# Optimization experiments

Hardware: AMD Instinct MI355X
Metric: run time of the kernel (lower is better)

Reference implementation:

```python
import jax, jax.numpy as jnp
import numpy as np

B, H, W, C, NH = 128, 14, 14, 768, 12
HD = C // NH  # 64
L = 2 * H - 1  # 27, rel pos table length


def setup_inputs() -> dict:
    key = jax.random.key(0)
    ks = jax.random.split(key, 6)
    return {
        "hidden_states": jax.random.normal(ks[0], (B, H, W, C), jnp.float32),
        "w_qkv": jax.random.normal(ks[1], (C, 3 * C), jnp.float32) * 0.02,
        "b_qkv": jnp.zeros((3 * C,), jnp.float32),
        "rel_pos_h": jax.random.normal(ks[2], (L, HD), jnp.float32) * 0.02,
        "rel_pos_w": jax.random.normal(ks[3], (L, HD), jnp.float32) * 0.02,
        "w_proj": jax.random.normal(ks[4], (C, C), jnp.float32) * 0.02,
        "b_proj": jnp.zeros((C,), jnp.float32),
    }


def _rel_table(size, rel_pos):
    # q_size == k_size -> coords = q - k + (size - 1), pure gather (no resize)
    coords = jnp.arange(size)[:, None] - jnp.arange(size)[None, :] + (size - 1)
    return rel_pos[coords]  # (size, size, HD)


def reference(hidden_states, w_qkv, b_qkv, rel_pos_h, rel_pos_w, w_proj, b_proj):
    scale = HD ** -0.5
    x = hidden_states.reshape(B, H * W, C)
    qkv = x @ w_qkv + b_qkv                                    # (B, HW, 3C)
    qkv = qkv.reshape(B, H * W, 3, NH, HD)
    qkv = jnp.transpose(qkv, (2, 0, 3, 1, 4)).reshape(3, B * NH, H * W, HD)
    q, k, v = qkv[0], qkv[1], qkv[2]                           # (B*NH, HW, HD)

    attn = jnp.einsum('bqd,bkd->bqk', q * scale, k)            # (B*NH, HW, HW)

    Rh = _rel_table(H, rel_pos_h)                              # (H, H, HD)
    Rw = _rel_table(W, rel_pos_w)                              # (W, W, HD)
    qr = q.reshape(B * NH, H, W, HD)
    rel_h = jnp.einsum('bhwc,hkc->bhwk', qr, Rh)               # (B*NH, H, W, H)
    rel_w = jnp.einsum('bhwc,wkc->bhwk', qr, Rw)               # (B*NH, H, W, W)

    attn = attn.reshape(B * NH, H, W, H, W)
    attn = attn + rel_h[..., :, None] + rel_w[..., None, :]
    attn = attn.reshape(B * NH, H * W, H * W)
    attn = jax.nn.softmax(attn, axis=-1)

    out = attn @ v                                             # (B*NH, HW, HD)
    out = out.reshape(B, NH, H, W, HD)
    out = jnp.transpose(out, (0, 2, 3, 1, 4)).reshape(B, H, W, C)
    return out @ w_proj + b_proj
```

## Files before the change

kernel.cpp:

```cpp
#include <hip/hip_runtime.h>

typedef __bf16 bf16_t;
typedef __bf16 bf16x8 __attribute__((ext_vector_type(8)));
typedef float floatx4 __attribute__((ext_vector_type(4)));

#define B_    128
#define H_    14
#define HW_   196
#define C_    768
#define NH_   12
#define HD_   64
#define M_    25088
#define NQKV_ 2304
#define KDIM_ 768
#define BK_   64
#define VPAD_ 208
#define RSTR  72
#define QSTR  104
#define PSTR  232
#define VSTR  224

__device__ __forceinline__ void async_cp16(const void* g, void* l) {
    __builtin_amdgcn_global_load_lds((const __attribute__((address_space(1))) void*)g,
                                     (__attribute__((address_space(3))) void*)l, 16, 0, 0);
}

__global__ __launch_bounds__(256) void cast_x_kernel(const float* __restrict__ in,
                                                     bf16_t* __restrict__ out) {
    size_t i = ((size_t)blockIdx.x * 256 + threadIdx.x) * 8;
    float4 a = *(const float4*)(in + i);
    float4 b = *(const float4*)(in + i + 4);
    bf16x8 v;
    v[0] = (bf16_t)a.x; v[1] = (bf16_t)a.y; v[2] = (bf16_t)a.z; v[3] = (bf16_t)a.w;
    v[4] = (bf16_t)b.x; v[5] = (bf16_t)b.y; v[6] = (bf16_t)b.z; v[7] = (bf16_t)b.w;
    *(bf16x8*)(out + i) = v;
}

__global__ __launch_bounds__(256) void transpose_cast_kernel(const float* __restrict__ in,
                                                             bf16_t* __restrict__ out,
                                                             int rows, int cols) {
    __shared__ float tile[32][33];
    int c0 = blockIdx.x * 32, r0 = blockIdx.y * 32;
    for (int i = threadIdx.y; i < 32; i += 8) {
        int r = r0 + i, c = c0 + threadIdx.x;
        if (r < rows && c < cols) tile[i][threadIdx.x] = in[(size_t)r * cols + c];
    }
    __syncthreads();
    for (int i = threadIdx.y; i < 32; i += 8) {
        int orow = c0 + i;
        int oc   = r0 + threadIdx.x;
        if (orow < cols && oc < rows)
            out[(size_t)orow * rows + oc] = (bf16_t)tile[threadIdx.x][i];
    }
}

__device__ __forceinline__ void gemm128_compute(const bf16_t* __restrict__ A,
                                                const bf16_t* __restrict__ Bt,
                                                int m0, int n0,
                                                floatx4 acc[4][4],
                                                bf16_t (*As)[BK_], bf16_t (*Bs)[BK_]) {
    const int tid  = threadIdx.x;
    const int lane = tid & 63, wave = tid >> 6;
    const int wm = (wave & 1) << 6, wn = (wave >> 1) << 6;
    const int lrow = lane & 15, quad = lane >> 4;

    #pragma unroll
    for (int i = 0; i < 4; i++)
        #pragma unroll
        for (int j = 0; j < 4; j++) acc[i][j] = (floatx4){0.f, 0.f, 0.f, 0.f};

    const int sr = tid >> 3;
    const int cc = tid & 7;

    for (int k0 = 0; k0 < KDIM_; k0 += BK_) {
        __syncthreads();
        #pragma unroll
        for (int i = 0; i < 4; i++) {
            int row  = sr + i * 32;
            int scol = ((cc ^ (row & 7)) * 8);
            async_cp16(A  + (size_t)(m0 + row) * KDIM_ + k0 + scol, &As[row][cc * 8]);
            async_cp16(Bt + (size_t)(n0 + row) * KDIM_ + k0 + scol, &Bs[row][cc * 8]);
        }
        __syncthreads();

        #pragma unroll
        for (int kh = 0; kh < 2; kh++) {
            bf16x8 af[4], bfr[4];
            #pragma unroll
            for (int i = 0; i < 4; i++) {
                int rw = wm + i * 16 + lrow;
                af[i] = *(const bf16x8*)&As[rw][((kh * 4 + quad) ^ (rw & 7)) * 8];
            }
            #pragma unroll
            for (int j = 0; j < 4; j++) {
                int rw = wn + j * 16 + lrow;
                bfr[j] = *(const bf16x8*)&Bs[rw][((kh * 4 + quad) ^ (rw & 7)) * 8];
            }
            #pragma unroll
            for (int i = 0; i < 4; i++)
                #pragma unroll
                for (int j = 0; j < 4; j++)
                    acc[i][j] = __builtin_amdgcn_mfma_f32_16x16x32_bf16(af[i], bfr[j], acc[i][j], 0, 0, 0);
        }
    }
}

__global__ __launch_bounds__(256) void qkv_gemm_kernel(const bf16_t* __restrict__ A,
                                                       const bf16_t* __restrict__ Bt,
                                                       const float* __restrict__ bias,
                                                       bf16_t* __restrict__ qb,
                                                       bf16_t* __restrict__ kb,
                                                       bf16_t* __restrict__ vtb) {
    __shared__ __align__(16) char smem[128 * 136 * 2];
    bf16_t (*As)[BK_] = (bf16_t(*)[BK_])smem;
    bf16_t (*Bs)[BK_] = (bf16_t(*)[BK_])(smem + 128 * BK_ * 2);
    bf16_t (*Cs)[136] = (bf16_t(*)[136])smem;

    const int lin = blockIdx.x;
    const int g = lin / 72, r = lin - g * 72;
    const int m0 = (g * 4 + (r & 3)) * 128;
    const int n0 = (r >> 2) * 128;
    floatx4 acc[4][4];
    gemm128_compute(A, Bt, m0, n0, acc, As, Bs);

    const int tid = threadIdx.x;
    const int lane = tid & 63, wave = tid >> 6;
    const int wm = (wave & 1) << 6, wn = (wave >> 1) << 6;
    const int lrow = lane & 15, quad = lane >> 4;
    const int sel = n0 / C_;

    if (sel == 2) {
        #pragma unroll
        for (int j = 0; j < 4; j++) {
            int n = n0 + wn + j * 16 + lrow;
            float bv = bias[n];
            int nc = n - 2 * C_;
            int nh = nc >> 6, hd = nc & 63;
            #pragma unroll
            for (int i = 0; i < 4; i++) {
                int m = m0 + wm + i * 16 + quad * 4;
                int b = m / HW_, t = m - b * HW_;
                int head = b * NH_ + nh;
                ushort4 pk;
                bf16_t h;
                h = (bf16_t)(acc[i][j][0] + bv); pk.x = __builtin_bit_cast(unsigned short, h);
                h = (bf16_t)(acc[i][j][1] + bv); pk.y = __builtin_bit_cast(unsigned short, h);
                h = (bf16_t)(acc[i][j][2] + bv); pk.z = __builtin_bit_cast(unsigned short, h);
                h = (bf16_t)(acc[i][j][3] + bv); pk.w = __builtin_bit_cast(unsigned short, h);
                *(ushort4*)(vtb + ((size_t)head * HD_ + hd) * VPAD_ + t) = pk;
            }
        }
    } else {
        const float sc = (sel == 0) ? 0.125f : 1.0f;
        __syncthreads();
        #pragma unroll
        for (int j = 0; j < 4; j++) {
            int n = n0 + wn + j * 16 + lrow;
            float bv = bias[n];
            #pragma unroll
            for (int i = 0; i < 4; i++)
                #pragma unroll
                for (int rr = 0; rr < 4; rr++)
                    Cs[wm + i * 16 + quad * 4 + rr][wn + j * 16 + lrow] =
                        (bf16_t)((acc[i][j][rr] + bv) * sc);
        }
        __syncthreads();
        bf16_t* dst = sel ? kb : qb;
        const int n0s = n0 - sel * C_;
        #pragma unroll
        for (int u = 0; u < 8; u++) {
            int idx = tid + u * 256;
            int rr = idx >> 4, c = idx & 15;
            int m = m0 + rr;
            int b = m / HW_, t = m - b * HW_;
            int ncol = n0s + c * 8;
            int nh = ncol >> 6, hd = ncol & 63;
            *(uint4*)(dst + (((size_t)(b * NH_ + nh)) * HW_ + t) * HD_ + hd) =
                *(const uint4*)&Cs[rr][c * 8];
        }
    }
}

__global__ __launch_bounds__(256) void proj_gemm_kernel(const bf16_t* __restrict__ A,
                                                        const bf16_t* __restrict__ Bt,
                                                        const float* __restrict__ bias,
                                                        float* __restrict__ out) {
    __shared__ __align__(16) bf16_t As[128][BK_];
    __shared__ __align__(16) bf16_t Bs[128][BK_];
    const int lin = blockIdx.x;
    const int g = lin / 24, r = lin - g * 24;
    const int m0 = (g * 4 + (r & 3)) * 128;
    const int n0 = (r >> 2) * 128;
    floatx4 acc[4][4];
    gemm128_compute(A, Bt, m0, n0, acc, As, Bs);

    const int lane = threadIdx.x & 63, wave = threadIdx.x >> 6;
    const int wm = (wave & 1) << 6, wn = (wave >> 1) << 6;
    const int lrow = lane & 15, quad = lane >> 4;
    #pragma unroll
    for (int j = 0; j < 4; j++) {
        int n = n0 + wn + j * 16 + lrow;
        float bv = bias[n];
        #pragma unroll
        for (int i = 0; i < 4; i++) {
            #pragma unroll
            for (int rr = 0; rr < 4; rr++) {
                int m = m0 + wm + i * 16 + quad * 4 + rr;
                out[(size_t)m * C_ + n] = acc[i][j][rr] + bv;
            }
        }
    }
}

__global__ __launch_bounds__(256, 3) void attn_kernel(const bf16_t* __restrict__ qb,
                                                      const bf16_t* __restrict__ kb,
                                                      const bf16_t* __restrict__ vtb,
                                                      const float* __restrict__ rph,
                                                      const float* __restrict__ rpw,
                                                      bf16_t* __restrict__ aout) {
    const int lin = blockIdx.x;
    const int task = (lin & 7) * 1344 + (lin >> 3);
    const int head = task / 7;
    const int qt = task - head * 7;
    const int bb = head / NH_, nh = head - bb * NH_;
    const int q0 = qt * 32;
    const int tid = threadIdx.x;
    const int lane = tid & 63, wave = tid >> 6;
    const int lrow = lane & 15, quad = lane >> 4;

    __shared__ __align__(16) bf16_t qs[32][QSTR];
    __shared__ __align__(16) bf16_t kvu[208 * QSTR];
    __shared__ __align__(16) bf16_t pbu[32 * PSTR];
    __shared__ bf16_t QRh[32][34];
    __shared__ bf16_t QRw[32][34];
    __shared__ float pmax[2][32], psum[2][32];

    bf16_t (*ks)[QSTR]  = (bf16_t(*)[QSTR])kvu;
    bf16_t (*vTs)[VSTR] = (bf16_t(*)[VSTR])kvu;
    bf16_t (*pb)[PSTR]  = (bf16_t(*)[PSTR])pbu;
    bf16_t (*rT)[RSTR]  = (bf16_t(*)[RSTR])pbu;

    bf16x8 z;
    #pragma unroll
    for (int e = 0; e < 8; e++) z[e] = (bf16_t)0.f;

    {
        int row = tid >> 3, col = (tid & 7) * 8;
        int t = q0 + row;
        *(bf16x8*)&qs[row][col] =
            (t < HW_) ? *(const bf16x8*)(qb + ((size_t)head * HW_ + t) * HD_ + col) : z;
    }
    #pragma unroll
    for (int t2 = 0; t2 < 2; t2++) {
        int u = tid * 2 + t2;
        int which = u >> 8, rem = u & 255;
        int l = rem >> 3, c = (rem & 7) * 8;
        bf16x8 v = z;
        if (l < 27) {
            const float* src = (which ? rpw : rph) + (size_t)l * HD_ + c;
            float4 a = *(const float4*)src;
            float4 b = *(const float4*)(src + 4);
            v[0] = (bf16_t)a.x; v[1] = (bf16_t)a.y; v[2] = (bf16_t)a.z; v[3] = (bf16_t)a.w;
            v[4] = (bf16_t)b.x; v[5] = (bf16_t)b.y; v[6] = (bf16_t)b.z; v[7] = (bf16_t)b.w;
        }
        *(bf16x8*)&rT[which * 32 + l][c] = v;
    }
    for (int v8 = tid; v8 < 208 * 8; v8 += 256) {
        int row = v8 >> 3, col = (v8 & 7) * 8;
        *(bf16x8*)&ks[row][col] =
            (row < HW_) ? *(const bf16x8*)(kb + ((size_t)head * HW_ + row) * HD_ + col) : z;
    }
    for (int u = tid; u < 208 * 5; u += 256) {
        int row = u / 5, c = u - row * 5;
        *(bf16x8*)&ks[row][64 + c * 8] = z;
    }
    __syncthreads();
    if (tid < 208 && tid < HW_) {
        int kh = tid / 14, kw = tid - kh * 14;
        ks[tid][64 + kh] = (bf16_t)1.0f;
        ks[tid][78 + kw] = (bf16_t)1.0f;
    }

    #pragma unroll
    for (int t2 = 0; t2 < 2; t2++) {
        int tsk = wave * 2 + t2;
        int which = tsk >> 2, mi2 = (tsk >> 1) & 1, ni = tsk & 1;
        floatx4 a4 = (floatx4){0.f, 0.f, 0.f, 0.f};
        #pragma unroll
        for (int kk = 0; kk < 2; kk++) {
            bf16x8 af  = *(const bf16x8*)&qs[mi2 * 16 + lrow][kk * 32 + quad * 8];
            bf16x8 bf8 = *(const bf16x8*)&rT[which * 32 + ni * 16 + lrow][kk * 32 + quad * 8];
            a4 = __builtin_amdgcn_mfma_f32_16x16x32_bf16(af, bf8, a4, 0, 0, 0);
        }
        int l = ni * 16 + lrow;
        if (l < 27) {
            bf16_t (*QR)[34] = which ? QRw : QRh;
            #pragma unroll
            for (int rr = 0; rr < 4; rr++) QR[mi2 * 16 + quad * 4 + rr][l] = (bf16_t)(a4[rr] * 8.f);
        }
    }
    __syncthreads();

    for (int u = tid; u < 1024; u += 256) {
        int row = u >> 5, kk = u & 31;
        int t = q0 + row;
        int h = t / 14, w = t - h * 14;
        bf16_t val = (bf16_t)0.f;
        if (kk < 14)      val = QRh[row][h - kk + 13];
        else if (kk < 28) val = QRw[row][w - (kk - 14) + 13];
        qs[row][64 + kk] = val;
    }
    if (tid < 96) {
        int row = tid / 3, col = 208 + (tid % 3) * 8;
        *(bf16x8*)&pb[row][col] = z;
    }
    __syncthreads();

    bf16x8 vstage[7];
    int vrow[7], vcol[7];
    #pragma unroll
    for (int i = 0; i < 7; i++) {
        int v8 = tid + i * 256;
        vrow[i] = v8 / 28;
        int c8 = v8 - vrow[i] * 28;
        vcol[i] = c8 * 8;
        vstage[i] = (vcol[i] < VPAD_)
            ? *(const bf16x8*)(vtb + ((size_t)head * HD_ + vrow[i]) * VPAD_ + vcol[i]) : z;
    }

    const int wh = wave >> 1, mi = wave & 1;
    const int NT = 7 - wh;
    float sv[7][4];
    float m4[4] = {-1e30f, -1e30f, -1e30f, -1e30f};
    for (int t = 0; t < NT; t++) {
        int jt = 2 * t + wh;
        floatx4 a4 = (floatx4){0.f, 0.f, 0.f, 0.f};
        #pragma unroll
        for (int kk = 0; kk < 3; kk++) {
            bf16x8 af  = *(const bf16x8*)&qs[mi * 16 + lrow][kk * 32 + quad * 8];
            bf16x8 bf8 = *(const bf16x8*)&ks[jt * 16 + lrow][kk * 32 + quad * 8];
            a4 = __builtin_amdgcn_mfma_f32_16x16x32_bf16(af, bf8, a4, 0, 0, 0);
        }
        int n = jt * 16 + lrow;
        bool valid = (n < HW_);
        #pragma unroll
        for (int rr = 0; rr < 4; rr++) {
            float s = valid ? a4[rr] : -1e30f;
            sv[t][rr] = s;
            m4[rr] = fmaxf(m4[rr], s);
        }
    }
    #pragma unroll
    for (int off = 1; off < 16; off <<= 1)
        #pragma unroll
        for (int rr = 0; rr < 4; rr++) m4[rr] = fmaxf(m4[rr], __shfl_xor(m4[rr], off));
    if (lrow == 0)
        #pragma unroll
        for (int rr = 0; rr < 4; rr++) pmax[wh][mi * 16 + quad * 4 + rr] = m4[rr];
    __syncthreads();

    float mxr[4], s4[4] = {0.f, 0.f, 0.f, 0.f};
    #pragma unroll
    for (int rr = 0; rr < 4; rr++) {
        int qi = mi * 16 + quad * 4 + rr;
        mxr[rr] = fmaxf(pmax[0][qi], pmax[1][qi]);
    }
    for (int t = 0; t < NT; t++) {
        int n = (2 * t + wh) * 16 + lrow;
        #pragma unroll
        for (int rr = 0; rr < 4; rr++) {
            float e = __expf(sv[t][rr] - mxr[rr]);
            s4[rr] += e;
            pb[mi * 16 + quad * 4 + rr][n] = (bf16_t)e;
        }
    }
    #pragma unroll
    for (int off = 1; off < 16; off <<= 1)
        #pragma unroll
        for (int rr = 0; rr < 4; rr++) s4[rr] += __shfl_xor(s4[rr], off);
    if (lrow == 0)
        #pragma unroll
        for (int rr = 0; rr < 4; rr++) psum[wh][mi * 16 + quad * 4 + rr] = s4[rr];
    #pragma unroll
    for (int i = 0; i < 7; i++) *(bf16x8*)&vTs[vrow[i]][vcol[i]] = vstage[i];
    __syncthreads();

    const int qit = wave & 1;
    const int qrow = qit * 16 + lrow;
    const float inv = 1.f / (psum[0][qrow] + psum[1][qrow]);
    const int t_out = q0 + qrow;
    #pragma unroll
    for (int jj = 0; jj < 2; jj++) {
        int hdt = (wave >> 1) * 2 + jj;
        floatx4 a4 = (floatx4){0.f, 0.f, 0.f, 0.f};
        #pragma unroll
        for (int kk = 0; kk < 7; kk++) {
            bf16x8 af  = *(const bf16x8*)&vTs[hdt * 16 + lrow][kk * 32 + quad * 8];
            bf16x8 bf8 = *(const bf16x8*)&pb[qit * 16 + lrow][kk * 32 + quad * 8];
            a4 = __builtin_amdgcn_mfma_f32_16x16x32_bf16(af, bf8, a4, 0, 0, 0);
        }
        if (t_out < HW_) {
            int col = nh * HD_ + hdt * 16 + quad * 4;
            ushort4 pk;
            bf16_t hv;
            hv = (bf16_t)(a4[0] * inv); pk.x = __builtin_bit_cast(unsigned short, hv);
            hv = (bf16_t)(a4[1] * inv); pk.y = __builtin_bit_cast(unsigned short, hv);
            hv = (bf16_t)(a4[2] * inv); pk.z = __builtin_bit_cast(unsigned short, hv);
            hv = (bf16_t)(a4[3] * inv); pk.w = __builtin_bit_cast(unsigned short, hv);
            *(ushort4*)(aout + ((size_t)bb * HW_ + t_out) * C_ + col) = pk;
        }
    }
}

extern "C" void kernel_launch(void* const* d_in, const int* in_sizes, int n_in,
                              void* d_out, int out_size, void* d_ws, size_t ws_size,
                              hipStream_t stream) {
    const float* hs    = (const float*)d_in[0];
    const float* wqkv  = (const float*)d_in[1];
    const float* bqkv  = (const float*)d_in[2];
    const float* rph   = (const float*)d_in[3];
    const float* rpw   = (const float*)d_in[4];
    const float* wproj = (const float*)d_in[5];
    const float* bproj = (const float*)d_in[6];
    float* out = (float*)d_out;

    char* ws = (char*)d_ws;
    bf16_t* x_bf   = (bf16_t*)(ws + 0);
    bf16_t* aout   = x_bf;
    bf16_t* wqkvT  = (bf16_t*)(ws + 38535168);
    bf16_t* wprojT = (bf16_t*)(ws + 42074112);
    bf16_t* qb     = (bf16_t*)(ws + 43253760);
    bf16_t* kb     = (bf16_t*)(ws + 81788928);
    bf16_t* vtb    = (bf16_t*)(ws + 120324096);

    cast_x_kernel<<<9408, 256, 0, stream>>>(hs, x_bf);
    transpose_cast_kernel<<<dim3(72, 24), dim3(32, 8), 0, stream>>>(wqkv, wqkvT, 768, 2304);
    transpose_cast_kernel<<<dim3(24, 24), dim3(32, 8), 0, stream>>>(wproj, wprojT, 768, 768);
    qkv_gemm_kernel<<<3528, 256, 0, stream>>>(x_bf, wqkvT, bqkv, qb, kb, vtb);
    attn_kernel<<<10752, 256, 0, stream>>>(qb, kb, vtb, rph, rpw, aout);
    proj_gemm_kernel<<<1176, 256, 0, stream>>>(aout, wprojT, bproj, out);
}
```

Measured before the change: 483.4 us.

## Process all query tiles per head in one block, keeping K and V resident

The attention kernel now launches one block per (batch, head) instead of one block per 32-row query tile. Each block loops over the seven query tiles, so K is staged in shared memory once and V is held in registers once per head rather than reloaded per tile. The next Q tile is prefetched into registers during the PV step. A new kernel zeroes the V padding columns up front, and occupancy is lowered to 2 blocks per CU. The trade is far fewer blocks (1536) with a longer serial loop each, which may hurt latency hiding and load balance.

New measurement: 411.0 us. 15.0% less time.

```diff
diff --git a/kernel.cpp b/kernel.cpp
--- a/kernel.cpp
+++ b/kernel.cpp
@@ -1,6 +1,7 @@
 #include <hip/hip_runtime.h>
 
 typedef __bf16 bf16_t;
+typedef __bf16 bf16x4 __attribute__((ext_vector_type(4)));
 typedef __bf16 bf16x8 __attribute__((ext_vector_type(8)));
 typedef float floatx4 __attribute__((ext_vector_type(4)));
 
@@ -18,7 +19,6 @@
 #define RSTR  72
 #define QSTR  104
 #define PSTR  232
-#define VSTR  224
 
 __device__ __forceinline__ void async_cp16(const void* g, void* l) {
     __builtin_amdgcn_global_load_lds((const __attribute__((address_space(1))) void*)g,
@@ -34,6 +34,15 @@
     v[0] = (bf16_t)a.x; v[1] = (bf16_t)a.y; v[2] = (bf16_t)a.z; v[3] = (bf16_t)a.w;
     v[4] = (bf16_t)b.x; v[5] = (bf16_t)b.y; v[6] = (bf16_t)b.z; v[7] = (bf16_t)b.w;
     *(bf16x8*)(out + i) = v;
+}
+
+__global__ __launch_bounds__(256) void zero_vpad_kernel(bf16_t* __restrict__ vtb) {
+    int row = blockIdx.x * 256 + threadIdx.x;
+    if (row < B_ * NH_ * HD_) {
+        bf16_t* p = vtb + (size_t)row * VPAD_ + HW_;
+        #pragma unroll
+        for (int i = 0; i < 12; i++) p[i] = (bf16_t)0.f;
+    }
 }
 
 __global__ __launch_bounds__(256) void transpose_cast_kernel(const float* __restrict__ in,
@@ -212,44 +221,30 @@
     }
 }
 
-__global__ __launch_bounds__(256, 3) void attn_kernel(const bf16_t* __restrict__ qb,
+__global__ __launch_bounds__(256, 2) void attn_kernel(const bf16_t* __restrict__ qb,
                                                       const bf16_t* __restrict__ kb,
                                                       const bf16_t* __restrict__ vtb,
                                                       const float* __restrict__ rph,
                                                       const float* __restrict__ rpw,
                                                       bf16_t* __restrict__ aout) {
-    const int lin = blockIdx.x;
-    const int task = (lin & 7) * 1344 + (lin >> 3);
-    const int head = task / 7;
-    const int qt = task - head * 7;
+    const int head = blockIdx.x;
     const int bb = head / NH_, nh = head - bb * NH_;
-    const int q0 = qt * 32;
     const int tid = threadIdx.x;
     const int lane = tid & 63, wave = tid >> 6;
     const int lrow = lane & 15, quad = lane >> 4;
 
     __shared__ __align__(16) bf16_t qs[32][QSTR];
-    __shared__ __align__(16) bf16_t kvu[208 * QSTR];
-    __shared__ __align__(16) bf16_t pbu[32 * PSTR];
+    __shared__ __align__(16) bf16_t ks[208][QSTR];
+    __shared__ __align__(16) bf16_t pb[32][PSTR];
+    __shared__ __align__(16) bf16_t rT[64][RSTR];
     __shared__ bf16_t QRh[32][34];
     __shared__ bf16_t QRw[32][34];
     __shared__ float pmax[2][32], psum[2][32];
 
-    bf16_t (*ks)[QSTR]  = (bf16_t(*)[QSTR])kvu;
-    bf16_t (*vTs)[VSTR] = (bf16_t(*)[VSTR])kvu;
-    bf16_t (*pb)[PSTR]  = (bf16_t(*)[PSTR])pbu;
-    bf16_t (*rT)[RSTR]  = (bf16_t(*)[RSTR])pbu;
-
     bf16x8 z;
     #pragma unroll
     for (int e = 0; e < 8; e++) z[e] = (bf16_t)0.f;
 
-    {
-        int row = tid >> 3, col = (tid & 7) * 8;
-        int t = q0 + row;
-        *(bf16x8*)&qs[row][col] =
-            (t < HW_) ? *(const bf16x8*)(qb + ((size_t)head * HW_ + t) * HD_ + col) : z;
-    }
     #pragma unroll
     for (int t2 = 0; t2 < 2; t2++) {
         int u = tid * 2 + t2;
@@ -274,140 +269,170 @@
         int row = u / 5, c = u - row * 5;
         *(bf16x8*)&ks[row][64 + c * 8] = z;
     }
+
+    bf16x8 vfr[2][7];
+    #pragma unroll
+    for (int jj = 0; jj < 2; jj++) {
+        int hdt = (wave >> 1) * 2 + jj;
+        #pragma unroll
+        for (int kk = 0; kk < 7; kk++) {
+            int col = kk * 32 + quad * 8;
+            bool ok = (col < VPAD_);
+            bf16x8 t = *(const bf16x8*)(vtb + ((size_t)head * HD_ + hdt * 16 + lrow) * VPAD_
+                                        + (ok ? col : 0));
+            vfr[jj][kk] = ok ? t : z;
+        }
+    }
+
+    const int qrow_st = tid >> 3, qcol_st = (tid & 7) * 8;
+    bf16x8 qreg = *(const bf16x8*)(qb + ((size_t)head * HW_ + qrow_st) * HD_ + qcol_st);
+
     __syncthreads();
-    if (tid < 208 && tid < HW_) {
+    if (tid < HW_) {
         int kh = tid / 14, kw = tid - kh * 14;
         ks[tid][64 + kh] = (bf16_t)1.0f;
         ks[tid][78 + kw] = (bf16_t)1.0f;
     }
-
-    #pragma unroll
-    for (int t2 = 0; t2 < 2; t2++) {
-        int tsk = wave * 2 + t2;
-        int which = tsk >> 2, mi2 = (tsk >> 1) & 1, ni = tsk & 1;
-        floatx4 a4 = (floatx4){0.f, 0.f, 0.f, 0.f};
-        #pragma unroll
-        for (int kk = 0; kk < 2; kk++) {
-            bf16x8 af  = *(const bf16x8*)&qs[mi2 * 16 + lrow][kk * 32 + quad * 8];
-            bf16x8 bf8 = *(const bf16x8*)&rT[which * 32 + ni * 16 + lrow][kk * 32 + quad * 8];
-            a4 = __builtin_amdgcn_mfma_f32_16x16x32_bf16(af, bf8, a4, 0, 0, 0);
-        }
-        int l = ni * 16 + lrow;
-        if (l < 27) {
-            bf16_t (*QR)[34] = which ? QRw : QRh;
-            #pragma unroll
-            for (int rr = 0; rr < 4; rr++) QR[mi2 * 16 + quad * 4 + rr][l] = (bf16_t)(a4[rr] * 8.f);
-        }
-    }
-    __syncthreads();
-
-    for (int u = tid; u < 1024; u += 256) {
-        int row = u >> 5, kk = u & 31;
-        int t = q0 + row;
-        int h = t / 14, w = t - h * 14;
-        bf16_t val = (bf16_t)0.f;
-        if (kk < 14)      val = QRh[row][h - kk + 13];
-        else if (kk < 28) val = QRw[row][w - (kk - 14) + 13];
-        qs[row][64 + kk] = val;
-    }
     if (tid < 96) {
         int row = tid / 3, col = 208 + (tid % 3) * 8;
         *(bf16x8*)&pb[row][col] = z;
     }
-    __syncthreads();
-
-    bf16x8 vstage[7];
-    int vrow[7], vcol[7];
-    #pragma unroll
-    for (int i = 0; i < 7; i++) {
-        int v8 = tid + i * 256;
-        vrow[i] = v8 / 28;
-        int c8 = v8 - vrow[i] * 28;
-        vcol[i] = c8 * 8;
-        vstage[i] = (vcol[i] < VPAD_)
-            ? *(const bf16x8*)(vtb + ((size_t)head * HD_ + vrow[i]) * VPAD_ + vcol[i]) : z;
-    }
 
     const int wh = wave >> 1, mi = wave & 1;
-    const int NT = 7 - wh;
-    float sv[7][4];
-    float m4[4] = {-1e30f, -1e30f, -1e30f, -1e30f};
-    for (int t = 0; t < NT; t++) {
-        int jt = 2 * t + wh;
-        floatx4 a4 = (floatx4){0.f, 0.f, 0.f, 0.f};
-        #pragma unroll
-        for (int kk = 0; kk < 3; kk++) {
-            bf16x8 af  = *(const bf16x8*)&qs[mi * 16 + lrow][kk * 32 + quad * 8];
-            bf16x8 bf8 = *(const bf16x8*)&ks[jt * 16 + lrow][kk * 32 + quad * 8];
-            a4 = __builtin_amdgcn_mfma_f32_16x16x32_bf16(af, bf8, a4, 0, 0, 0);
-        }
-        int n = jt * 16 + lrow;
-        bool valid = (n < HW_);
+    const int qit = wave & 1;
+
+    for (int qt = 0; qt < 7; qt++) {
+        const int q0 = qt * 32;
+
+        *(bf16x8*)&qs[qrow_st][qcol_st] = qreg;
+        __syncthreads();
+
+        #pragma unroll
+        for (int t2 = 0; t2 < 2; t2++) {
+            int tsk = wave * 2 + t2;
+            int which = tsk >> 2, mi2 = (tsk >> 1) & 1, ni = tsk & 1;
+            floatx4 a4 = (floatx4){0.f, 0.f, 0.f, 0.f};
+            #pragma unroll
+            for (int kk = 0; kk < 2; kk++) {
+                bf16x8 af  = *(const bf16x8*)&qs[mi2 * 16 + lrow][kk * 32 + quad * 8];
+                bf16x8 bf8 = *(const bf16x8*)&rT[which * 32 + ni * 16 + lrow][kk * 32 + quad * 8];
+                a4 = __builtin_amdgcn_mfma_f32_16x16x32_bf16(af, bf8, a4, 0, 0, 0);
+            }
+            int l = ni * 16 + lrow;
+            if (l < 27) {
+                bf16_t (*QR)[34] = which ? QRw : QRh;
+                #pragma unroll
+                for (int rr = 0; rr < 4; rr++) QR[mi2 * 16 + quad * 4 + rr][l] = (bf16_t)(a4[rr] * 8.f);
+            }
+        }
+        __syncthreads();
+
+        {
+            int row = tid >> 3;
+            int kk4 = (tid & 7) * 4;
+            int t = q0 + row;
+            int h = t / 14, w = t - h * 14;
+            bf16x4 pk;
+            #pragma unroll
+            for (int s = 0; s < 4; s++) {
+                int kk = kk4 + s;
+                bf16_t val = (bf16_t)0.f;
+                if (kk < 14)      val = QRh[row][h - kk + 13];
+                else if (kk < 28) val = QRw[row][w - (kk - 14) + 13];
+                pk[s] = val;
+            }
+            *(bf16x4*)&qs[row][64 + kk4] = pk;
+        }
+        __syncthreads();
+
+        float sv[7][4];
+        float m4[4] = {-1e30f, -1e30f, -1e30f, -1e30f};
+        #pragma unroll
+        for (int t = 0; t < 7; t++) {
+            int jt = 2 * t + wh;
+            if (jt < 13) {
+                floatx4 a4 = (floatx4){0.f, 0.f, 0.f, 0.f};
+                #pragma unroll
+                for (int kk = 0; kk < 3; kk++) {
+                    bf16x8 af  = *(const bf16x8*)&qs[mi * 16 + lrow][kk * 32 + quad * 8];
+                    bf16x8 bf8 = *(const bf16x8*)&ks[jt * 16 + lrow][kk * 32 + quad * 8];
+                    a4 = __builtin_amdgcn_mfma_f32_16x16x32_bf16(af, bf8, a4, 0, 0, 0);
+                }
+                int n = jt * 16 + lrow;
+                bool valid = (n < HW_);
+                #pragma unroll
+                for (int rr = 0; rr < 4; rr++) {
+                    float s = valid ? a4[rr] : -1e30f;
+                    sv[t][rr] = s;
+                    m4[rr] = fmaxf(m4[rr], s);
+                }
+            }
+        }
+        #pragma unroll
+        for (int off = 1; off < 16; off <<= 1)
+            #pragma unroll
+            for (int rr = 0; rr < 4; rr++) m4[rr] = fmaxf(m4[rr], __shfl_xor(m4[rr], off));
+        if (lrow == 0)
+            #pragma unroll
+            for (int rr = 0; rr < 4; rr++) pmax[wh][mi * 16 + quad * 4 + rr] = m4[rr];
+        __syncthreads();
+
+        float mxr[4], s4[4] = {0.f, 0.f, 0.f, 0.f};
         #pragma unroll
         for (int rr = 0; rr < 4; rr++) {
-            float s = valid ? a4[rr] : -1e30f;
-            sv[t][rr] = s;
-            m4[rr] = fmaxf(m4[rr], s);
-        }
-    }
-    #pragma unroll
-    for (int off = 1; off < 16; off <<= 1)
-        #pragma unroll
-        for (int rr = 0; rr < 4; rr++) m4[rr] = fmaxf(m4[rr], __shfl_xor(m4[rr], off));
-    if (lrow == 0)
-        #pragma unroll
-        for (int rr = 0; rr < 4; rr++) pmax[wh][mi * 16 + quad * 4 + rr] = m4[rr];
-    __syncthreads();
-
-    float mxr[4], s4[4] = {0.f, 0.f, 0.f, 0.f};
-    #pragma unroll
-    for (int rr = 0; rr < 4; rr++) {
-        int qi = mi * 16 + quad * 4 + rr;
-        mxr[rr] = fmaxf(pmax[0][qi], pmax[1][qi]);
-    }
-    for (int t = 0; t < NT; t++) {
-        int n = (2 * t + wh) * 16 + lrow;
-        #pragma unroll
-        for (int rr = 0; rr < 4; rr++) {
-            float e = __expf(sv[t][rr] - mxr[rr]);
-            s4[rr] += e;
-            pb[mi * 16 + quad * 4 + rr][n] = (bf16_t)e;
-        }
-    }
-    #pragma unroll
-    for (int off = 1; off < 16; off <<= 1)
-        #pragma unroll
-        for (int rr = 0; rr < 4; rr++) s4[rr] += __shfl_xor(s4[rr], off);
-    if (lrow == 0)
-        #pragma unroll
-        for (int rr = 0; rr < 4; rr++) psum[wh][mi * 16 + quad * 4 + rr] = s4[rr];
-    #pragma unroll
-    for (int i = 0; i < 7; i++) *(bf16x8*)&vTs[vrow[i]][vcol[i]] = vstage[i];
-    __syncthreads();
-
-    const int qit = wave & 1;
-    const int qrow = qit * 16 + lrow;
-    const float inv = 1.f / (psum[0][qrow] + psum[1][qrow]);
-    const int t_out = q0 + qrow;
-    #pragma unroll
-    for (int jj = 0; jj < 2; jj++) {
-        int hdt = (wave >> 1) * 2 + jj;
-        floatx4 a4 = (floatx4){0.f, 0.f, 0.f, 0.f};
-        #pragma unroll
-        for (int kk = 0; kk < 7; kk++) {
-            bf16x8 af  = *(const bf16x8*)&vTs[hdt * 16 + lrow][kk * 32 + quad * 8];
-            bf16x8 bf8 = *(const bf16x8*)&pb[qit * 16 + lrow][kk * 32 + quad * 8];
-            a4 = __builtin_amdgcn_mfma_f32_16x16x32_bf16(af, bf8, a4, 0, 0, 0);
-        }
-        if (t_out < HW_) {
-            int col = nh * HD_ + hdt * 16 + quad * 4;
-            ushort4 pk;
-            bf16_t hv;
-            hv = (bf16_t)(a4[0] * inv); pk.x = __builtin_bit_cast(unsigned short, hv);
-            hv = (bf16_t)(a4[1] * inv); pk.y = __builtin_bit_cast(unsigned short, hv);
-            hv = (bf16_t)(a4[2] * inv); pk.z = __builtin_bit_cast(unsigned short, hv);
-            hv = (bf16_t)(a4[3] * inv); pk.w = __builtin_bit_cast(unsigned short, hv);
-            *(ushort4*)(aout + ((size_t)bb * HW_ + t_out) * C_ + col) = pk;
+            int qi = mi * 16 + quad * 4 + rr;
+            mxr[rr] = fmaxf(pmax[0][qi], pmax[1][qi]);
+        }
+        #pragma unroll
+        for (int t = 0; t < 7; t++) {
+            int jt = 2 * t + wh;
+            if (jt < 13) {
+                int n = jt * 16 + lrow;
+                #pragma unroll
+                for (int rr = 0; rr < 4; rr++) {
+                    float e = __expf(sv[t][rr] - mxr[rr]);
+                    s4[rr] += e;
+                    pb[mi * 16 + quad * 4 + rr][n] = (bf16_t)e;
+                }
+            }
+        }
+        #pragma unroll
+        for (int off = 1; off < 16; off <<= 1)
+            #pragma unroll
+            for (int rr = 0; rr < 4; rr++) s4[rr] += __shfl_xor(s4[rr], off);
+        if (lrow == 0)
+            #pragma unroll
+            for (int rr = 0; rr < 4; rr++) psum[wh][mi * 16 + quad * 4 + rr] = s4[rr];
+        __syncthreads();
+
+        const int qrow = qit * 16 + lrow;
+        const float inv = 1.f / (psum[0][qrow] + psum[1][qrow]);
+        const int t_out = q0 + qrow;
+
+        if (qt < 6) {
+            int t = q0 + 32 + qrow_st;
+            qreg = (t < HW_) ? *(const bf16x8*)(qb + ((size_t)head * HW_ + t) * HD_ + qcol_st) : z;
+        }
+
+        #pragma unroll
+        for (int jj = 0; jj < 2; jj++) {
+            int hdt = (wave >> 1) * 2 + jj;
+            floatx4 a4 = (floatx4){0.f, 0.f, 0.f, 0.f};
+            #pragma unroll
+            for (int kk = 0; kk < 7; kk++) {
+                bf16x8 bf8 = *(const bf16x8*)&pb[qit * 16 + lrow][kk * 32 + quad * 8];
+                a4 = __builtin_amdgcn_mfma_f32_16x16x32_bf16(vfr[jj][kk], bf8, a4, 0, 0, 0);
+            }
+            if (t_out < HW_) {
+                int col = nh * HD_ + hdt * 16 + quad * 4;
+                ushort4 pk;
+                bf16_t hv;
+                hv = (bf16_t)(a4[0] * inv); pk.x = __builtin_bit_cast(unsigned short, hv);
+                hv = (bf16_t)(a4[1] * inv); pk.y = __builtin_bit_cast(unsigned short, hv);
+                hv = (bf16_t)(a4[2] * inv); pk.z = __builtin_bit_cast(unsigned short, hv);
+                hv = (bf16_t)(a4[3] * inv); pk.w = __builtin_bit_cast(unsigned short, hv);
+                *(ushort4*)(aout + ((size_t)bb * HW_ + t_out) * C_ + col) = pk;
+            }
         }
     }
 }
@@ -434,9 +459,10 @@
     bf16_t* vtb    = (bf16_t*)(ws + 120324096);
 
     cast_x_kernel<<<9408, 256, 0, stream>>>(hs, x_bf);
+    zero_vpad_kernel<<<384, 256, 0, stream>>>(vtb);
     transpose_cast_kernel<<<dim3(72, 24), dim3(32, 8), 0, stream>>>(wqkv, wqkvT, 768, 2304);
     transpose_cast_kernel<<<dim3(24, 24), dim3(32, 8), 0, stream>>>(wproj, wprojT, 768, 768);
     qkv_gemm_kernel<<<3528, 256, 0, stream>>>(x_bf, wqkvT, bqkv, qb, kb, vtb);
-    attn_kernel<<<10752, 256, 0, stream>>>(qb, kb, vtb, rph, rpw, aout);
+    attn_kernel<<<B_ * NH_, 256, 0, stream>>>(qb, kb, vtb, rph, rpw, aout);
     proj_gemm_kernel<<<1176, 256, 0, stream>>>(aout, wprojT, bproj, out);
 }
```
